# Kernel tuning notes

Measured on AMD Instinct MI355X. Metric: run time of the kernel, lower is better.

Reference implementation:

```python
import jax, jax.numpy as jnp
import numpy as np

# Architecture constants (match init_kwargs)
A = 4            # num_areas
E_PER = 512      # excitatory units per area
I_PER = 128      # inhibitory units per area
H = A * (E_PER + I_PER)   # 2560 hidden units, order: [all E (area-major), all I]
NUM_OBJS = 2
IN_UNITS = 64
IN = NUM_OBJS * IN_UNITS  # 128 input units
DT, TAU_X = 0.02, 0.1
ALPHA_X = DT / TAU_X


def _build_masks():
    """Signed Dale's-law connectivity masks, as in _get_connectivity_mask_* ."""
    # inter-area recurrent connectivity: nearest-neighbor hierarchy + self
    rec = np.eye(A) + np.eye(A, k=1) + np.eye(A, k=-1)
    ee = np.kron(rec, np.ones((E_PER, E_PER)))
    ei = np.kron(np.eye(A), np.ones((E_PER, I_PER)))   # E<-I only within area
    ie = np.kron(rec, np.ones((I_PER, E_PER)))
    ii = np.kron(np.eye(A), np.ones((I_PER, I_PER)))
    conn = np.block([[ee, ei], [ie, ii]])
    # sign mask: first e_size columns excitatory (+1), rest inhibitory (-1)
    sign = np.concatenate([np.ones(A * E_PER), -np.ones(A * I_PER)])[None, :]
    rec_mask = conn * sign
    np.fill_diagonal(rec_mask, 0.0)  # remove_diag=True in h2h EILinear
    # input mask: only area 0 receives external input; e_prop=1 for x2h (all +1)
    in_area = np.zeros((A, NUM_OBJS)); in_area[0, :] = 1.0
    in_e = np.kron(in_area, np.ones((E_PER, IN_UNITS)))
    in_i = np.kron(in_area, np.ones((I_PER, IN_UNITS)))
    in_mask = np.concatenate([in_e, in_i], axis=0)
    return jnp.asarray(rec_mask, jnp.float32), jnp.asarray(in_mask, jnp.float32)


def setup_inputs() -> dict:
    key = jax.random.key(0)
    k1, k2, k3 = jax.random.split(key, 3)
    T, B = 500, 64
    inputs = jax.random.normal(k1, (T, B, IN), dtype=jnp.float32)
    W_rec = jax.random.normal(k2, (H, H), dtype=jnp.float32) / np.sqrt(H)
    b_rec = jnp.zeros((H,), dtype=jnp.float32)
    W_in = jax.random.normal(k3, (H, IN), dtype=jnp.float32) / np.sqrt(IN)
    return {"inputs": inputs, "W_rec": W_rec, "b_rec": b_rec, "W_in": W_in}


def reference(inputs, W_rec, b_rec, W_in):
    rec_mask, in_mask = _build_masks()
    # EILinear effective weights: pos_func=abs, times signed connectivity mask
    W_rec_eff = jnp.abs(W_rec) * rec_mask          # [H, H]
    W_in_eff = jnp.abs(W_in) * in_mask             # [H, IN]
    # input projection for all timesteps at once
    proj = jnp.einsum('tbi,hi->tbh', inputs, W_in_eff)  # [T, B, H]

    def retanh(x):
        return jnp.tanh(jax.nn.relu(x))

    def step(carry, u_t):
        x, r = carry
        pre = r @ W_rec_eff.T + b_rec + u_t        # h2h(r) + x2h(u)
        x = (1.0 - ALPHA_X) * x + ALPHA_X * pre    # leaky integration
        r = retanh(x)
        return (x, r), r

    B = inputs.shape[1]
    x0 = jnp.zeros((B, H), dtype=inputs.dtype)     # x0 (train_init_state=False)
    (_, _), rates = jax.lax.scan(step, (x0, retanh(x0)), proj)
    return rates  # [T, B, H] firing rates
```

## Files before the change

### kernel.cpp

```cpp
#include <hip/hip_runtime.h>
#include <math.h>

#define Hn   2560
#define Bn   64
#define INW  128
#define ETOT 2048
#define HGn  160
#define MAXC 13

typedef __attribute__((ext_vector_type(8))) _Float16 half8;
typedef __attribute__((ext_vector_type(4))) float  floatx4;

__global__ void build_apack(const float* __restrict__ Wrec,
                            const float* __restrict__ Win,
                            _Float16* __restrict__ Af) {
  int hg = blockIdx.x, c = blockIdx.y;
  int a = (hg < 128) ? (hg >> 5) : ((hg - 128) >> 3);
  int nE = (a == 0 || a == 3) ? 8 : 12;
  int nch = nE + 1 + (a == 0 ? 1 : 0);
  if (c >= nch) return;
  int h0 = hg * 16;
  int tid = threadIdx.x;
  int kq = tid >> 6, L = tid & 63;
  int m = L & 15, q = L >> 4;
  int h = h0 + m;

  const float* src; int k0, stride; float sgn; bool isIn = false;
  if (c < nE)       { k0 = ((a == 0 ? 0 : a - 1) << 9) + (c << 7); src = Wrec; stride = Hn;  sgn =  1.f; }
  else if (c == nE) { k0 = ETOT + (a << 7);                        src = Wrec; stride = Hn;  sgn = -1.f; }
  else              { k0 = 0;                                      src = Win;  stride = INW; sgn =  1.f; isIn = true; }

  _Float16 hi8[8], lo8[8];
  #pragma unroll
  for (int j = 0; j < 8; ++j) {
    int k = k0 + kq * 32 + q * 8 + j;
    float w = fabsf(src[(size_t)h * stride + k]);
    if (!isIn && k == h) w = 0.f;
    w *= sgn;
    _Float16 wh = (_Float16)w;
    hi8[j] = wh;
    lo8[j] = (_Float16)(w - (float)wh);
  }
  _Float16* outp = Af + (size_t)(hg * MAXC + c) * 4096;
  *(uint4*)(outp + (kq * 2 + 0) * 512 + L * 8) = *(const uint4*)hi8;
  *(uint4*)(outp + (kq * 2 + 1) * 512 + L * 8) = *(const uint4*)lo8;
}

__global__ __launch_bounds__(512) void rnn_step(
    const _Float16* __restrict__ Af,
    const float* __restrict__ inputs,
    const _Float16* __restrict__ rf, _Float16* __restrict__ rfD,
    const float* __restrict__ brec,
    float* __restrict__ xT, float* __restrict__ rates, int t)
{
  __shared__ float red[8][1056];
  __shared__ float rrt[16][68];
  __shared__ float bb[16];

  int hg  = blockIdx.x;
  int tid = threadIdx.x;
  int w   = tid >> 6, L = tid & 63;
  int h0  = hg * 16;
  int a   = (hg < 128) ? (hg >> 5) : ((hg - 128) >> 3);
  int nE  = (a == 0 || a == 3) ? 8 : 12;
  int nch = nE + 1 + (a == 0 ? 1 : 0);
  int SK  = nch * 4;
  int ktE0 = (a == 0 ? 0 : a - 1) * 16;
  int ktI0 = 64 + a * 4;

  if (tid < 16) bb[tid] = brec[h0 + tid];
  __syncthreads();

  const _Float16* Abase = Af + (size_t)hg * MAXC * 4096;

  floatx4 ac0 = {0.f,0.f,0.f,0.f}, ac1 = {0.f,0.f,0.f,0.f};
  floatx4 ac2 = {0.f,0.f,0.f,0.f}, ac3 = {0.f,0.f,0.f,0.f};

  for (int ks = w; ks < SK; ks += 8) {
    int c = ks >> 2, kq = ks & 3;
    const _Float16* Ap = Abase + (size_t)c * 4096 + (size_t)(kq * 2) * 512 + L * 8;
    half8 ah = *(const half8*)Ap;
    half8 al = *(const half8*)(Ap + 512);
    half8 b0, b1, b2, b3;
    if (c <= nE) {
      int kt = (c < nE) ? (ktE0 + c * 4 + kq) : (ktI0 + kq);
      const _Float16* Bp = rf + (size_t)kt * 2048 + L * 8;
      b0 = *(const half8*)(Bp);
      b1 = *(const half8*)(Bp + 512);
      b2 = *(const half8*)(Bp + 1024);
      b3 = *(const half8*)(Bp + 1536);
    } else {
      const float* ip = inputs + (size_t)t * (Bn * INW) + kq * 32 + (L >> 4) * 8;
      int nb = L & 15;
      #pragma unroll
      for (int j = 0; j < 8; ++j) b0[j] = (_Float16)ip[(nb +  0) * INW + j];
      #pragma unroll
      for (int j = 0; j < 8; ++j) b1[j] = (_Float16)ip[(nb + 16) * INW + j];
      #pragma unroll
      for (int j = 0; j < 8; ++j) b2[j] = (_Float16)ip[(nb + 32) * INW + j];
      #pragma unroll
      for (int j = 0; j < 8; ++j) b3[j] = (_Float16)ip[(nb + 48) * INW + j];
    }
    ac0 = __builtin_amdgcn_mfma_f32_16x16x32_f16(ah, b0, ac0, 0, 0, 0);
    ac0 = __builtin_amdgcn_mfma_f32_16x16x32_f16(al, b0, ac0, 0, 0, 0);
    ac1 = __builtin_amdgcn_mfma_f32_16x16x32_f16(ah, b1, ac1, 0, 0, 0);
    ac1 = __builtin_amdgcn_mfma_f32_16x16x32_f16(al, b1, ac1, 0, 0, 0);
    ac2 = __builtin_amdgcn_mfma_f32_16x16x32_f16(ah, b2, ac2, 0, 0, 0);
    ac2 = __builtin_amdgcn_mfma_f32_16x16x32_f16(al, b2, ac2, 0, 0, 0);
    ac3 = __builtin_amdgcn_mfma_f32_16x16x32_f16(ah, b3, ac3, 0, 0, 0);
    ac3 = __builtin_amdgcn_mfma_f32_16x16x32_f16(al, b3, ac3, 0, 0, 0);
  }

  #pragma unroll
  for (int p = 0; p < 4; ++p) {
    int m = (L >> 4) * 4 + p;
    float* rw = &red[w][m * 66 + (L & 15)];
    rw[ 0] = ac0[p];
    rw[16] = ac1[p];
    rw[32] = ac2[p];
    rw[48] = ac3[p];
  }
  __syncthreads();

  #pragma unroll
  for (int e = 0; e < 2; ++e) {
    int elem = tid + e * 512;
    int m = elem >> 6, n = elem & 63;
    float s = 0.f;
    #pragma unroll
    for (int j = 0; j < 8; ++j) s += red[j][m * 66 + n];
    size_t xi = (size_t)(h0 + m) * 64 + n;
    float x = xT[xi];
    x = 0.8f * x + 0.2f * (s + bb[m]);
    xT[xi] = x;
    rrt[m][n] = tanhf(fmaxf(x, 0.f));
  }
  __syncthreads();

  if (tid < 128) {
    int bt = tid >> 5, Lq = tid & 31;
    int Lp = (hg & 1) * 32 + Lq;
    _Float16 v8[8];
    #pragma unroll
    for (int j = 0; j < 8; ++j)
      v8[j] = (_Float16)rrt[(Lq >> 4) * 8 + j][bt * 16 + (Lq & 15)];
    *(uint4*)(rfD + (size_t)((hg >> 1) * 4 + bt) * 512 + Lp * 8) = *(const uint4*)v8;
  }
  if (tid >= 256) {
    int tt = tid - 256;
    int b = tt >> 2, hq = tt & 3;
    float4 o = make_float4(rrt[hq * 4 + 0][b], rrt[hq * 4 + 1][b],
                           rrt[hq * 4 + 2][b], rrt[hq * 4 + 3][b]);
    *(float4*)(rates + (size_t)t * (Bn * Hn) + (size_t)b * Hn + h0 + hq * 4) = o;
  }
}

extern "C" void kernel_launch(void* const* d_in, const int* in_sizes, int n_in,
                              void* d_out, int out_size, void* d_ws, size_t ws_size,
                              hipStream_t stream) {
  const float* inputs = (const float*)d_in[0];
  const float* Wrec   = (const float*)d_in[1];
  const float* brec   = (const float*)d_in[2];
  const float* Win    = (const float*)d_in[3];
  int T = in_sizes[0] / (Bn * INW);

  char* base = (char*)d_ws;
  size_t off = 0;
  _Float16* Af  = (_Float16*)(base + off); off += (size_t)HGn * MAXC * 4096 * 2;
  _Float16* rfA = (_Float16*)(base + off); off += (size_t)80 * 4 * 512 * 2;
  _Float16* rfB = (_Float16*)(base + off); off += (size_t)80 * 4 * 512 * 2;
  float*    xT  = (float*)(base + off);    off += (size_t)Hn * Bn * 4;

  hipMemsetAsync(rfA, 0, (size_t)80 * 4 * 512 * 2, stream);
  hipMemsetAsync(xT,  0, (size_t)Hn * Bn * 4, stream);

  build_apack<<<dim3(HGn, MAXC), 256, 0, stream>>>(Wrec, Win, Af);

  float* rates = (float*)d_out;
  for (int t = 0; t < T; ++t) {
    const _Float16* rs = (t & 1) ? rfB : rfA;
    _Float16*       rd = (t & 1) ? rfA : rfB;
    rnn_step<<<HGn, 512, 0, stream>>>(Af, inputs, rs, rd, brec, xT, rates, t);
  }
}
```

Measured before the change: 3.330 ms.

## Replace per-timestep launches with persistent kernel and grid-wide atomic barrier

```diff
diff --git a/kernel.cpp b/kernel.cpp
--- a/kernel.cpp
+++ b/kernel.cpp
@@ -7,6 +7,8 @@
 #define ETOT 2048
 #define HGn  160
 #define MAXC 13
+#define NBLK 160
+#define MAXI 7
 
 typedef __attribute__((ext_vector_type(8))) _Float16 half8;
 typedef __attribute__((ext_vector_type(4))) float  floatx4;
@@ -46,112 +48,156 @@
   *(uint4*)(outp + (kq * 2 + 1) * 512 + L * 8) = *(const uint4*)lo8;
 }
 
-__global__ __launch_bounds__(512) void rnn_step(
+__global__ __launch_bounds__(512, 2) void rnn_persist(
     const _Float16* __restrict__ Af,
     const float* __restrict__ inputs,
-    const _Float16* __restrict__ rf, _Float16* __restrict__ rfD,
+    _Float16* __restrict__ rfA, _Float16* __restrict__ rfB,
     const float* __restrict__ brec,
-    float* __restrict__ xT, float* __restrict__ rates, int t)
+    float* __restrict__ rates,
+    unsigned* bcnt, unsigned* bgen, int T)
 {
   __shared__ float red[8][1056];
   __shared__ float rrt[16][68];
   __shared__ float bb[16];
 
-  int hg  = blockIdx.x;
-  int tid = threadIdx.x;
-  int w   = tid >> 6, L = tid & 63;
-  int h0  = hg * 16;
-  int a   = (hg < 128) ? (hg >> 5) : ((hg - 128) >> 3);
-  int nE  = (a == 0 || a == 3) ? 8 : 12;
-  int nch = nE + 1 + (a == 0 ? 1 : 0);
-  int SK  = nch * 4;
-  int ktE0 = (a == 0 ? 0 : a - 1) * 16;
-  int ktI0 = 64 + a * 4;
+  const int hg  = blockIdx.x;
+  const int tid = threadIdx.x;
+  const int w   = tid >> 6, L = tid & 63;
+  const int h0  = hg * 16;
+  const int a   = (hg < 128) ? (hg >> 5) : ((hg - 128) >> 3);
+  const int nE  = (a == 0 || a == 3) ? 8 : 12;
+  const int SK  = (nE + 1 + (a == 0 ? 1 : 0)) * 4;
+  const int ktE0 = (a == 0 ? 0 : a - 1) * 16;
+  const int ktI0 = 64 + a * 4;
 
   if (tid < 16) bb[tid] = brec[h0 + tid];
+
+  half8 ah[MAXI], al[MAXI];
+  int   boff[MAXI];
+  bool  act[MAXI], isin[MAXI];
+  const _Float16* Abase = Af + (size_t)hg * MAXC * 4096;
+  #pragma unroll
+  for (int i = 0; i < MAXI; ++i) {
+    int ks = w + i * 8;
+    act[i]  = ks < SK;
+    isin[i] = false;
+    boff[i] = 0;
+    if (act[i]) {
+      int c = ks >> 2, kq = ks & 3;
+      const _Float16* Ap = Abase + (size_t)c * 4096 + (size_t)(kq * 2) * 512 + (size_t)L * 8;
+      ah[i] = *(const half8*)Ap;
+      al[i] = *(const half8*)(Ap + 512);
+      if (c <= nE) {
+        int kt = (c < nE) ? (ktE0 + c * 4 + kq) : (ktI0 + kq);
+        boff[i] = kt * 2048 + L * 8;
+      } else {
+        isin[i] = true;
+        boff[i] = kq * 32 + (L >> 4) * 8;
+      }
+    }
+  }
+
+  float xv[2] = {0.f, 0.f};
+
   __syncthreads();
 
-  const _Float16* Abase = Af + (size_t)hg * MAXC * 4096;
-
-  floatx4 ac0 = {0.f,0.f,0.f,0.f}, ac1 = {0.f,0.f,0.f,0.f};
-  floatx4 ac2 = {0.f,0.f,0.f,0.f}, ac3 = {0.f,0.f,0.f,0.f};
-
-  for (int ks = w; ks < SK; ks += 8) {
-    int c = ks >> 2, kq = ks & 3;
-    const _Float16* Ap = Abase + (size_t)c * 4096 + (size_t)(kq * 2) * 512 + L * 8;
-    half8 ah = *(const half8*)Ap;
-    half8 al = *(const half8*)(Ap + 512);
-    half8 b0, b1, b2, b3;
-    if (c <= nE) {
-      int kt = (c < nE) ? (ktE0 + c * 4 + kq) : (ktI0 + kq);
-      const _Float16* Bp = rf + (size_t)kt * 2048 + L * 8;
-      b0 = *(const half8*)(Bp);
-      b1 = *(const half8*)(Bp + 512);
-      b2 = *(const half8*)(Bp + 1024);
-      b3 = *(const half8*)(Bp + 1536);
-    } else {
-      const float* ip = inputs + (size_t)t * (Bn * INW) + kq * 32 + (L >> 4) * 8;
-      int nb = L & 15;
+  for (int t = 0; t < T; ++t) {
+    const _Float16* __restrict__ rs = (t & 1) ? rfB : rfA;
+    _Float16* __restrict__ rd       = (t & 1) ? rfA : rfB;
+
+    floatx4 ac0 = {0.f,0.f,0.f,0.f}, ac1 = {0.f,0.f,0.f,0.f};
+    floatx4 ac2 = {0.f,0.f,0.f,0.f}, ac3 = {0.f,0.f,0.f,0.f};
+
+    #pragma unroll
+    for (int i = 0; i < MAXI; ++i) {
+      if (!act[i]) continue;
+      half8 b0, b1, b2, b3;
+      if (isin[i]) {
+        const float* ip = inputs + (size_t)t * (Bn * INW) + boff[i];
+        int nb = L & 15;
+        #pragma unroll
+        for (int j = 0; j < 8; ++j) b0[j] = (_Float16)ip[(nb +  0) * INW + j];
+        #pragma unroll
+        for (int j = 0; j < 8; ++j) b1[j] = (_Float16)ip[(nb + 16) * INW + j];
+        #pragma unroll
+        for (int j = 0; j < 8; ++j) b2[j] = (_Float16)ip[(nb + 32) * INW + j];
+        #pragma unroll
+        for (int j = 0; j < 8; ++j) b3[j] = (_Float16)ip[(nb + 48) * INW + j];
+      } else {
+        const _Float16* Bp = rs + boff[i];
+        b0 = *(const half8*)(Bp);
+        b1 = *(const half8*)(Bp + 512);
+        b2 = *(const half8*)(Bp + 1024);
+        b3 = *(const half8*)(Bp + 1536);
+      }
+      ac0 = __builtin_amdgcn_mfma_f32_16x16x32_f16(ah[i], b0, ac0, 0, 0, 0);
+      ac0 = __builtin_amdgcn_mfma_f32_16x16x32_f16(al[i], b0, ac0, 0, 0, 0);
+      ac1 = __builtin_amdgcn_mfma_f32_16x16x32_f16(ah[i], b1, ac1, 0, 0, 0);
+      ac1 = __builtin_amdgcn_mfma_f32_16x16x32_f16(al[i], b1, ac1, 0, 0, 0);
+      ac2 = __builtin_amdgcn_mfma_f32_16x16x32_f16(ah[i], b2, ac2, 0, 0, 0);
+      ac2 = __builtin_amdgcn_mfma_f32_16x16x32_f16(al[i], b2, ac2, 0, 0, 0);
+      ac3 = __builtin_amdgcn_mfma_f32_16x16x32_f16(ah[i], b3, ac3, 0, 0, 0);
+      ac3 = __builtin_amdgcn_mfma_f32_16x16x32_f16(al[i], b3, ac3, 0, 0, 0);
+    }
+
+    #pragma unroll
+    for (int p = 0; p < 4; ++p) {
+      int m = (L >> 4) * 4 + p;
+      float* rw = &red[w][m * 66 + (L & 15)];
+      rw[ 0] = ac0[p];
+      rw[16] = ac1[p];
+      rw[32] = ac2[p];
+      rw[48] = ac3[p];
+    }
+    __syncthreads();
+
+    #pragma unroll
+    for (int e = 0; e < 2; ++e) {
+      int elem = tid + e * 512;
+      int m = elem >> 6, n = elem & 63;
+      float s = 0.f;
       #pragma unroll
-      for (int j = 0; j < 8; ++j) b0[j] = (_Float16)ip[(nb +  0) * INW + j];
+      for (int j = 0; j < 8; ++j) s += red[j][m * 66 + n];
+      float x = 0.8f * xv[e] + 0.2f * (s + bb[m]);
+      xv[e] = x;
+      rrt[m][n] = tanhf(fmaxf(x, 0.f));
+    }
+    __syncthreads();
+
+    if (tid < 128) {
+      int bt = tid >> 5, Lq = tid & 31;
+      int Lp = (hg & 1) * 32 + Lq;
+      _Float16 v8[8];
       #pragma unroll
-      for (int j = 0; j < 8; ++j) b1[j] = (_Float16)ip[(nb + 16) * INW + j];
-      #pragma unroll
-      for (int j = 0; j < 8; ++j) b2[j] = (_Float16)ip[(nb + 32) * INW + j];
-      #pragma unroll
-      for (int j = 0; j < 8; ++j) b3[j] = (_Float16)ip[(nb + 48) * INW + j];
-    }
-    ac0 = __builtin_amdgcn_mfma_f32_16x16x32_f16(ah, b0, ac0, 0, 0, 0);
-    ac0 = __builtin_amdgcn_mfma_f32_16x16x32_f16(al, b0, ac0, 0, 0, 0);
-    ac1 = __builtin_amdgcn_mfma_f32_16x16x32_f16(ah, b1, ac1, 0, 0, 0);
-    ac1 = __builtin_amdgcn_mfma_f32_16x16x32_f16(al, b1, ac1, 0, 0, 0);
-    ac2 = __builtin_amdgcn_mfma_f32_16x16x32_f16(ah, b2, ac2, 0, 0, 0);
-    ac2 = __builtin_amdgcn_mfma_f32_16x16x32_f16(al, b2, ac2, 0, 0, 0);
-    ac3 = __builtin_amdgcn_mfma_f32_16x16x32_f16(ah, b3, ac3, 0, 0, 0);
-    ac3 = __builtin_amdgcn_mfma_f32_16x16x32_f16(al, b3, ac3, 0, 0, 0);
-  }
-
-  #pragma unroll
-  for (int p = 0; p < 4; ++p) {
-    int m = (L >> 4) * 4 + p;
-    float* rw = &red[w][m * 66 + (L & 15)];
-    rw[ 0] = ac0[p];
-    rw[16] = ac1[p];
-    rw[32] = ac2[p];
-    rw[48] = ac3[p];
-  }
-  __syncthreads();
-
-  #pragma unroll
-  for (int e = 0; e < 2; ++e) {
-    int elem = tid + e * 512;
-    int m = elem >> 6, n = elem & 63;
-    float s = 0.f;
-    #pragma unroll
-    for (int j = 0; j < 8; ++j) s += red[j][m * 66 + n];
-    size_t xi = (size_t)(h0 + m) * 64 + n;
-    float x = xT[xi];
-    x = 0.8f * x + 0.2f * (s + bb[m]);
-    xT[xi] = x;
-    rrt[m][n] = tanhf(fmaxf(x, 0.f));
-  }
-  __syncthreads();
-
-  if (tid < 128) {
-    int bt = tid >> 5, Lq = tid & 31;
-    int Lp = (hg & 1) * 32 + Lq;
-    _Float16 v8[8];
-    #pragma unroll
-    for (int j = 0; j < 8; ++j)
-      v8[j] = (_Float16)rrt[(Lq >> 4) * 8 + j][bt * 16 + (Lq & 15)];
-    *(uint4*)(rfD + (size_t)((hg >> 1) * 4 + bt) * 512 + Lp * 8) = *(const uint4*)v8;
-  }
-  if (tid >= 256) {
-    int tt = tid - 256;
-    int b = tt >> 2, hq = tt & 3;
-    float4 o = make_float4(rrt[hq * 4 + 0][b], rrt[hq * 4 + 1][b],
-                           rrt[hq * 4 + 2][b], rrt[hq * 4 + 3][b]);
-    *(float4*)(rates + (size_t)t * (Bn * Hn) + (size_t)b * Hn + h0 + hq * 4) = o;
+      for (int j = 0; j < 8; ++j)
+        v8[j] = (_Float16)rrt[(Lq >> 4) * 8 + j][bt * 16 + (Lq & 15)];
+      *(uint4*)(rd + (size_t)((hg >> 1) * 4 + bt) * 512 + (size_t)Lp * 8) = *(const uint4*)v8;
+    }
+    if (tid >= 256) {
+      int tt = tid - 256;
+      int b = tt >> 2, hq = tt & 3;
+      float4 o = make_float4(rrt[hq * 4 + 0][b], rrt[hq * 4 + 1][b],
+                             rrt[hq * 4 + 2][b], rrt[hq * 4 + 3][b]);
+      *(float4*)(rates + (size_t)t * (Bn * Hn) + (size_t)b * Hn + h0 + hq * 4) = o;
+    }
+    __syncthreads();
+
+    if (tid == 0) {
+      __threadfence();
+      unsigned arr = atomicAdd(bcnt, 1u);
+      unsigned tgt = (unsigned)NBLK * (unsigned)(t + 1);
+      if (arr == tgt - 1u) {
+        __hip_atomic_store(bgen, (unsigned)(t + 1),
+                           __ATOMIC_RELEASE, __HIP_MEMORY_SCOPE_AGENT);
+      } else {
+        while (__hip_atomic_load(bgen, __ATOMIC_RELAXED,
+                                 __HIP_MEMORY_SCOPE_AGENT) < (unsigned)(t + 1)) {
+          __builtin_amdgcn_s_sleep(2);
+        }
+      }
+      __threadfence();
+    }
+    __syncthreads();
   }
 }
 
@@ -169,17 +215,14 @@
   _Float16* Af  = (_Float16*)(base + off); off += (size_t)HGn * MAXC * 4096 * 2;
   _Float16* rfA = (_Float16*)(base + off); off += (size_t)80 * 4 * 512 * 2;
   _Float16* rfB = (_Float16*)(base + off); off += (size_t)80 * 4 * 512 * 2;
-  float*    xT  = (float*)(base + off);    off += (size_t)Hn * Bn * 4;
+  unsigned* bar = (unsigned*)(base + off); off += 512;
 
   hipMemsetAsync(rfA, 0, (size_t)80 * 4 * 512 * 2, stream);
-  hipMemsetAsync(xT,  0, (size_t)Hn * Bn * 4, stream);
+  hipMemsetAsync(bar, 0, 512, stream);
 
   build_apack<<<dim3(HGn, MAXC), 256, 0, stream>>>(Wrec, Win, Af);
 
   float* rates = (float*)d_out;
-  for (int t = 0; t < T; ++t) {
-    const _Float16* rs = (t & 1) ? rfB : rfA;
-    _Float16*       rd = (t & 1) ? rfA : rfB;
-    rnn_step<<<HGn, 512, 0, stream>>>(Af, inputs, rs, rd, brec, xT, rates, t);
-  }
+  rnn_persist<<<NBLK, 512, 0, stream>>>(Af, inputs, rfA, rfB, brec, rates,
+                                        bar, bar + 64, T);
 }
```

New measurement: 6.026 ms. 1.81x slower.
